# Performance work log

Hardware: AMD Instinct MI355X
Metric: run time of the kernel (lower is better)

## Reference

```python
import jax, jax.numpy as jnp
import numpy as np

# Module hyperparameters (init_kwargs)
D = 2          # input_dim
OUT = 3        # output_dim
T = 14         # log2 hash table size
L = 16         # number of levels
F = 2          # features per level
N_MIN, N_MAX = 16, 512
B = 1048576    # batch of query points
HIDDEN = 64

_b = np.exp((np.log(N_MAX) - np.log(N_MIN)) / (L - 1))
RES = jnp.asarray(np.floor(N_MIN * _b ** np.arange(L)).astype(np.float32))  # [L]

# voxel corner offsets [D, 2^D] (same construction as torch module)
_border = np.empty((D, 2 ** D), dtype=np.int32)
for _i in range(D):
    _border[_i, :] = np.array(([0] * 2 ** _i + [1] * 2 ** _i) * 2 ** (D - _i - 1), dtype=np.int32)
BORDER = jnp.asarray(_border)

# NVIDIA tiny-cuda-nn primes; uint32 arithmetic is exact for the low T bits
# (low 14 bits of a product/xor only depend on low 32 bits), matching torch's
# int64 multiply-xor followed by mod 2^T.
PRIMES = jnp.array([1, 2654435761, 805459861, 3674653429, 2097192037, 1434869437, 2165219737][:D], dtype=jnp.uint32)


def setup_inputs() -> dict:
    key = jax.random.key(0)
    ks = jax.random.split(key, 8)
    x = jax.random.uniform(ks[0], (B, D), jnp.float32)  # coords in [0,1)
    tables = jax.random.uniform(ks[1], (L, 2 ** T, F), jnp.float32, -1e-4, 1e-4)
    W1 = jax.random.normal(ks[2], (HIDDEN, L * F), jnp.float32) * 0.05
    b1 = jnp.zeros((HIDDEN,), jnp.float32)
    W2 = jax.random.normal(ks[3], (HIDDEN, HIDDEN), jnp.float32) * 0.05
    b2 = jnp.zeros((HIDDEN,), jnp.float32)
    W3 = jax.random.normal(ks[4], (OUT, HIDDEN), jnp.float32) * 0.05
    b3 = jnp.zeros((OUT,), jnp.float32)
    return {"x": x, "tables": tables, "W1": W1, "b1": b1, "W2": W2, "b2": b2, "W3": W3, "b3": b3}


def reference(x, tables, W1, b1, W2, b2, W3, b3):
    n = x.shape[0]
    # scale coords by each level resolution: [B, D, L]
    scaled = x[:, :, None] * RES[None, None, :]
    grid = jnp.floor(scaled).astype(jnp.int32)                     # [B, D, L]
    corners = grid[..., None] + BORDER[None, :, None, :]           # [B, D, L, 2^D]
    # spatial hash: xor of coord * prime per dimension, mod 2^T
    h = jnp.zeros((n, L, 2 ** D), jnp.uint32)
    for i in range(D):
        h = h ^ (corners[:, i].astype(jnp.uint32) * PRIMES[i])
    idx = (h & jnp.uint32(2 ** T - 1)).astype(jnp.int32)           # [B, L, 2^D]
    # per-level embedding gather: [B, L, 2^D, F]
    looked = tables[jnp.arange(L)[None, :, None], idx]
    # (bi/tri)linear interpolation weights: prod over dims -> [B, L, 2^D]
    w = jnp.prod(1.0 - jnp.abs(scaled[..., None] - corners.astype(x.dtype)), axis=1)
    feat = jnp.einsum('blc,blcf->blf', w, looked).reshape(n, L * F)  # [B, L*F]
    # small MLP head
    h1 = jax.nn.relu(feat @ W1.T + b1)
    h2 = jax.nn.relu(h1 @ W2.T + b2)
    return h2 @ W3.T + b3
```

## Files before the change

### kernel.cpp

```cpp
#include <hip/hip_runtime.h>
#include <hip/hip_bf16.h>
#include <math.h>


#define TBL_MASK 16383u
#define PRIME1   2654435761u

typedef __attribute__((ext_vector_type(8))) short short8;
typedef __attribute__((ext_vector_type(4))) float f32x4;
typedef __attribute__((ext_vector_type(4))) unsigned int uint4v;

struct ResArr { float r[16]; };

__device__ __forceinline__ unsigned short bf16rn(float f) {
    __hip_bfloat16 h = __float2bfloat16(f);
    return __builtin_bit_cast(unsigned short, h);
}
__device__ __forceinline__ float bf16tof(unsigned short u) {
    unsigned int x = ((unsigned int)u) << 16;
    return __builtin_bit_cast(float, x);
}

__device__ __forceinline__ void splitW(const float* __restrict__ p,
                                       short8& hi, short8& lo) {
    const float4 w0 = *(const float4*)p;
    const float4 w1 = *(const float4*)(p + 4);
    float v[8] = {w0.x, w0.y, w0.z, w0.w, w1.x, w1.y, w1.z, w1.w};
    #pragma unroll
    for (int e = 0; e < 8; ++e) {
        const unsigned short hb = bf16rn(v[e]);
        const unsigned short lb = bf16rn(v[e] - bf16tof(hb));
        hi[e] = (short)hb;
        lo[e] = (short)lb;
    }
}

__device__ __forceinline__ void splitWm(const float* __restrict__ p, bool valid,
                                        short8& hi, short8& lo) {
    float v[8];
    if (valid) {
        const float4 w0 = *(const float4*)p;
        const float4 w1 = *(const float4*)(p + 4);
        v[0] = w0.x; v[1] = w0.y; v[2] = w0.z; v[3] = w0.w;
        v[4] = w1.x; v[5] = w1.y; v[6] = w1.z; v[7] = w1.w;
    } else {
        #pragma unroll
        for (int e = 0; e < 8; ++e) v[e] = 0.0f;
    }
    #pragma unroll
    for (int e = 0; e < 8; ++e) {
        const unsigned short hb = bf16rn(v[e]);
        const unsigned short lb = bf16rn(v[e] - bf16tof(hb));
        hi[e] = (short)hb;
        lo[e] = (short)lb;
    }
}

__device__ __forceinline__ short8 ldsFrag(const unsigned short* p) {
    return __builtin_bit_cast(short8, *(const uint4v*)p);
}

#define MFMA(a, b, c) __builtin_amdgcn_mfma_f32_16x16x32_bf16((a), (b), (c), 0, 0, 0)

__global__ __launch_bounds__(64) void mh_mfma(
    const float* __restrict__ x,
    const float* __restrict__ tables,
    const float* __restrict__ W1,
    const float* __restrict__ b1,
    const float* __restrict__ W2,
    const float* __restrict__ b2,
    const float* __restrict__ W3,
    const float* __restrict__ b3,
    float* __restrict__ out,
    ResArr res, int n)
{
    __shared__ unsigned short sFH[64 * 40];
    __shared__ unsigned short sFL[64 * 40];
    __shared__ unsigned short sAH[32 * 72];
    __shared__ unsigned short sAL[32 * 72];

    const int L  = threadIdx.x;
    const int ln = L & 15;
    const int q  = L >> 4;
    const long base = (long)blockIdx.x * 64;
    long s = base + L;
    if (s >= (long)n) s = (long)n - 1;

    const float2 xv = reinterpret_cast<const float2*>(x)[s];
    const float2* __restrict__ tbl2 = reinterpret_cast<const float2*>(tables);

    #pragma unroll 4
    for (int l = 0; l < 16; ++l) {
        const float r  = res.r[l];
        const float sx = xv.x * r;
        const float sy = xv.y * r;
        const float gx = floorf(sx);
        const float gy = floorf(sy);
        const unsigned ux = (unsigned)(int)gx;
        const unsigned uy = (unsigned)(int)gy;
        const unsigned hy0 = uy * PRIME1;
        const unsigned hy1 = hy0 + PRIME1;
        const unsigned i00 = ( ux       ^ hy0) & TBL_MASK;
        const unsigned i10 = ((ux + 1u) ^ hy0) & TBL_MASK;
        const unsigned i01 = ( ux       ^ hy1) & TBL_MASK;
        const unsigned i11 = ((ux + 1u) ^ hy1) & TBL_MASK;
        const float2* tl = tbl2 + (l << 14);
        const float2 t00 = tl[i00];
        const float2 t10 = tl[i10];
        const float2 t01 = tl[i01];
        const float2 t11 = tl[i11];
        const float wx0 = 1.0f - fabsf(sx - gx);
        const float wx1 = 1.0f - fabsf(sx - (gx + 1.0f));
        const float wy0 = 1.0f - fabsf(sy - gy);
        const float wy1 = 1.0f - fabsf(sy - (gy + 1.0f));
        const float w00 = wx0 * wy0;
        const float w10 = wx1 * wy0;
        const float w01 = wx0 * wy1;
        const float w11 = wx1 * wy1;
        const float f0 = fmaf(w00, t00.x, fmaf(w10, t10.x, fmaf(w01, t01.x, w11 * t11.x)));
        const float f1 = fmaf(w00, t00.y, fmaf(w10, t10.y, fmaf(w01, t01.y, w11 * t11.y)));
        const unsigned short h0 = bf16rn(f0);
        const unsigned short h1e = bf16rn(f1);
        const unsigned short l0 = bf16rn(f0 - bf16tof(h0));
        const unsigned short l1 = bf16rn(f1 - bf16tof(h1e));
        *(unsigned int*)&sFH[L * 40 + 2 * l] = (unsigned)h0 | ((unsigned)h1e << 16);
        *(unsigned int*)&sFL[L * 40 + 2 * l] = (unsigned)l0 | ((unsigned)l1 << 16);
    }

    float b1v[4], b2v[4];
    #pragma unroll
    for (int nt = 0; nt < 4; ++nt) { b1v[nt] = b1[nt * 16 + ln]; b2v[nt] = b2[nt * 16 + ln]; }
    const float b3v = (ln < 3) ? b3[ln] : 0.0f;

    const f32x4 zero4 = {0.0f, 0.0f, 0.0f, 0.0f};

    for (int mh = 0; mh < 2; ++mh) {
        short8 a1h[2], a1l[2];
        #pragma unroll
        for (int mt = 0; mt < 2; ++mt) {
            const int row = mh * 32 + mt * 16 + ln;
            a1h[mt] = ldsFrag(&sFH[row * 40 + q * 8]);
            a1l[mt] = ldsFrag(&sFL[row * 40 + q * 8]);
        }
        f32x4 acc1[2][4];
        #pragma unroll
        for (int mt = 0; mt < 2; ++mt)
            #pragma unroll
            for (int nt = 0; nt < 4; ++nt) acc1[mt][nt] = zero4;

        #pragma unroll
        for (int nt = 0; nt < 4; ++nt) {
            short8 bh, bl;
            splitW(W1 + (nt * 16 + ln) * 32 + q * 8, bh, bl);
            #pragma unroll
            for (int mt = 0; mt < 2; ++mt) {
                f32x4 a = acc1[mt][nt];
                a = MFMA(a1l[mt], bh, a);
                a = MFMA(a1h[mt], bl, a);
                a = MFMA(a1h[mt], bh, a);
                acc1[mt][nt] = a;
            }
        }
        #pragma unroll
        for (int mt = 0; mt < 2; ++mt)
            #pragma unroll
            for (int nt = 0; nt < 4; ++nt) {
                const int col = nt * 16 + ln;
                #pragma unroll
                for (int r = 0; r < 4; ++r) {
                    float v = fmaxf(acc1[mt][nt][r] + b1v[nt], 0.0f);
                    const unsigned short hb = bf16rn(v);
                    const unsigned short lb = bf16rn(v - bf16tof(hb));
                    const int rl = mt * 16 + q * 4 + r;
                    sAH[rl * 72 + col] = hb;
                    sAL[rl * 72 + col] = lb;
                }
            }

        short8 a2h[2][2], a2l[2][2];
        #pragma unroll
        for (int mt = 0; mt < 2; ++mt)
            #pragma unroll
            for (int ks = 0; ks < 2; ++ks) {
                const int row = mt * 16 + ln;
                a2h[mt][ks] = ldsFrag(&sAH[row * 72 + ks * 32 + q * 8]);
                a2l[mt][ks] = ldsFrag(&sAL[row * 72 + ks * 32 + q * 8]);
            }
        f32x4 acc2[2][4];
        #pragma unroll
        for (int mt = 0; mt < 2; ++mt)
            #pragma unroll
            for (int nt = 0; nt < 4; ++nt) acc2[mt][nt] = zero4;

        #pragma unroll
        for (int nt = 0; nt < 4; ++nt)
            #pragma unroll
            for (int ks = 0; ks < 2; ++ks) {
                short8 bh, bl;
                splitW(W2 + (nt * 16 + ln) * 64 + ks * 32 + q * 8, bh, bl);
                #pragma unroll
                for (int mt = 0; mt < 2; ++mt) {
                    f32x4 a = acc2[mt][nt];
                    a = MFMA(a2l[mt][ks], bh, a);
                    a = MFMA(a2h[mt][ks], bl, a);
                    a = MFMA(a2h[mt][ks], bh, a);
                    acc2[mt][nt] = a;
                }
            }
        #pragma unroll
        for (int mt = 0; mt < 2; ++mt)
            #pragma unroll
            for (int nt = 0; nt < 4; ++nt) {
                const int col = nt * 16 + ln;
                #pragma unroll
                for (int r = 0; r < 4; ++r) {
                    float v = fmaxf(acc2[mt][nt][r] + b2v[nt], 0.0f);
                    const unsigned short hb = bf16rn(v);
                    const unsigned short lb = bf16rn(v - bf16tof(hb));
                    const int rl = mt * 16 + q * 4 + r;
                    sAH[rl * 72 + col] = hb;
                    sAL[rl * 72 + col] = lb;
                }
            }

        short8 a3h[2][2], a3l[2][2];
        #pragma unroll
        for (int mt = 0; mt < 2; ++mt)
            #pragma unroll
            for (int ks = 0; ks < 2; ++ks) {
                const int row = mt * 16 + ln;
                a3h[mt][ks] = ldsFrag(&sAH[row * 72 + ks * 32 + q * 8]);
                a3l[mt][ks] = ldsFrag(&sAL[row * 72 + ks * 32 + q * 8]);
            }
        f32x4 acc3[2] = {zero4, zero4};
        #pragma unroll
        for (int ks = 0; ks < 2; ++ks) {
            short8 bh, bl;
            splitWm(W3 + ln * 64 + ks * 32 + q * 8, ln < 3, bh, bl);
            #pragma unroll
            for (int mt = 0; mt < 2; ++mt) {
                f32x4 a = acc3[mt];
                a = MFMA(a3l[mt][ks], bh, a);
                a = MFMA(a3h[mt][ks], bl, a);
                a = MFMA(a3h[mt][ks], bh, a);
                acc3[mt] = a;
            }
        }
        if (ln < 3) {
            #pragma unroll
            for (int mt = 0; mt < 2; ++mt)
                #pragma unroll
                for (int r = 0; r < 4; ++r) {
                    const long sg = base + mh * 32 + mt * 16 + q * 4 + r;
                    if (sg < (long)n) out[sg * 3 + ln] = acc3[mt][r] + b3v;
                }
        }
    }
}

extern "C" void kernel_launch(void* const* d_in, const int* in_sizes, int n_in,
                              void* d_out, int out_size, void* d_ws, size_t ws_size,
                              hipStream_t stream) {
    const float* x      = (const float*)d_in[0];
    const float* tables = (const float*)d_in[1];
    const float* W1     = (const float*)d_in[2];
    const float* b1v    = (const float*)d_in[3];
    const float* W2     = (const float*)d_in[4];
    const float* b2v    = (const float*)d_in[5];
    const float* W3     = (const float*)d_in[6];
    const float* b3v    = (const float*)d_in[7];
    float* out = (float*)d_out;

    const int n = in_sizes[0] / 2;

    ResArr ra;
    const double bb = exp((log(512.0) - log(16.0)) / 15.0);
    for (int k = 0; k < 16; ++k) ra.r[k] = (float)floor(16.0 * pow(bb, (double)k));

    dim3 grid((n + 63) / 64), block(64);
    hipLaunchKernelGGL(mh_mfma, grid, block, 0, stream,
                       x, tables, W1, b1v, W2, b2v, W3, b3v, out, ra, n);
}
```

Baseline: 238.6 us.

## Pre-split MLP weights into bf16 hi/lo in a prep kernel

A small prep kernel now converts W1, W2 and W3 once per call into bf16 hi/lo pairs in workspace (W3 zero-padded to 16 rows). The main kernel then loads ready fragments instead of re-splitting the weights in every block, which removes a large amount of per-block VALU conversion work. Shared memory is aliased between the feature and activation buffers, with the feature fragments hoisted into registers beforehand. The encoding loop unroll is raised to 8. The cost is an extra launch and added register pressure.

Measured after the change: 255.7 us. 7.1% more time.

```diff
diff --git a/kernel.cpp b/kernel.cpp
--- a/kernel.cpp
+++ b/kernel.cpp
@@ -12,6 +12,13 @@
 
 struct ResArr { float r[16]; };
 
+#define WS_W1H 0
+#define WS_W1L 2048
+#define WS_W2H 4096
+#define WS_W2L 8192
+#define WS_W3H 12288
+#define WS_W3L 13312
+
 __device__ __forceinline__ unsigned short bf16rn(float f) {
     __hip_bfloat16 h = __float2bfloat16(f);
     return __builtin_bit_cast(unsigned short, h);
@@ -20,64 +27,54 @@
     unsigned int x = ((unsigned int)u) << 16;
     return __builtin_bit_cast(float, x);
 }
-
-__device__ __forceinline__ void splitW(const float* __restrict__ p,
-                                       short8& hi, short8& lo) {
-    const float4 w0 = *(const float4*)p;
-    const float4 w1 = *(const float4*)(p + 4);
-    float v[8] = {w0.x, w0.y, w0.z, w0.w, w1.x, w1.y, w1.z, w1.w};
-    #pragma unroll
-    for (int e = 0; e < 8; ++e) {
-        const unsigned short hb = bf16rn(v[e]);
-        const unsigned short lb = bf16rn(v[e] - bf16tof(hb));
-        hi[e] = (short)hb;
-        lo[e] = (short)lb;
+__device__ __forceinline__ short8 ldFrag(const unsigned short* p) {
+    return __builtin_bit_cast(short8, *(const uint4v*)p);
+}
+
+#define MFMA(a, b, c) __builtin_amdgcn_mfma_f32_16x16x32_bf16((a), (b), (c), 0, 0, 0)
+
+__global__ __launch_bounds__(256) void prep_weights(
+    const float* __restrict__ W1,
+    const float* __restrict__ W2,
+    const float* __restrict__ W3,
+    unsigned short* __restrict__ ws)
+{
+    const int t = blockIdx.x * 256 + threadIdx.x;
+    if (t < 2048) {
+        const float v = W1[t];
+        const unsigned short hb = bf16rn(v);
+        ws[WS_W1H + t] = hb;
+        ws[WS_W1L + t] = bf16rn(v - bf16tof(hb));
+    } else if (t < 2048 + 4096) {
+        const int i = t - 2048;
+        const float v = W2[i];
+        const unsigned short hb = bf16rn(v);
+        ws[WS_W2H + i] = hb;
+        ws[WS_W2L + i] = bf16rn(v - bf16tof(hb));
+    } else if (t < 2048 + 4096 + 1024) {
+        const int i = t - 6144;
+        const int r = i >> 6, c = i & 63;
+        const float v = (r < 3) ? W3[r * 64 + c] : 0.0f;
+        const unsigned short hb = bf16rn(v);
+        ws[WS_W3H + i] = hb;
+        ws[WS_W3L + i] = bf16rn(v - bf16tof(hb));
     }
 }
-
-__device__ __forceinline__ void splitWm(const float* __restrict__ p, bool valid,
-                                        short8& hi, short8& lo) {
-    float v[8];
-    if (valid) {
-        const float4 w0 = *(const float4*)p;
-        const float4 w1 = *(const float4*)(p + 4);
-        v[0] = w0.x; v[1] = w0.y; v[2] = w0.z; v[3] = w0.w;
-        v[4] = w1.x; v[5] = w1.y; v[6] = w1.z; v[7] = w1.w;
-    } else {
-        #pragma unroll
-        for (int e = 0; e < 8; ++e) v[e] = 0.0f;
-    }
-    #pragma unroll
-    for (int e = 0; e < 8; ++e) {
-        const unsigned short hb = bf16rn(v[e]);
-        const unsigned short lb = bf16rn(v[e] - bf16tof(hb));
-        hi[e] = (short)hb;
-        lo[e] = (short)lb;
-    }
-}
-
-__device__ __forceinline__ short8 ldsFrag(const unsigned short* p) {
-    return __builtin_bit_cast(short8, *(const uint4v*)p);
-}
-
-#define MFMA(a, b, c) __builtin_amdgcn_mfma_f32_16x16x32_bf16((a), (b), (c), 0, 0, 0)
 
 __global__ __launch_bounds__(64) void mh_mfma(
     const float* __restrict__ x,
     const float* __restrict__ tables,
-    const float* __restrict__ W1,
     const float* __restrict__ b1,
-    const float* __restrict__ W2,
     const float* __restrict__ b2,
-    const float* __restrict__ W3,
     const float* __restrict__ b3,
+    const unsigned short* __restrict__ ws,
     float* __restrict__ out,
     ResArr res, int n)
 {
-    __shared__ unsigned short sFH[64 * 40];
-    __shared__ unsigned short sFL[64 * 40];
-    __shared__ unsigned short sAH[32 * 72];
-    __shared__ unsigned short sAL[32 * 72];
+    __shared__ char smem[10240];
+    unsigned short* sF  = (unsigned short*)smem;
+    unsigned short* sAH = (unsigned short*)smem;
+    unsigned short* sAL = (unsigned short*)(smem + 4608);
 
     const int L  = threadIdx.x;
     const int ln = L & 15;
@@ -89,7 +86,7 @@
     const float2 xv = reinterpret_cast<const float2*>(x)[s];
     const float2* __restrict__ tbl2 = reinterpret_cast<const float2*>(tables);
 
-    #pragma unroll 4
+    #pragma unroll 8
     for (int l = 0; l < 16; ++l) {
         const float r  = res.r[l];
         const float sx = xv.x * r;
@@ -123,9 +120,19 @@
         const unsigned short h1e = bf16rn(f1);
         const unsigned short l0 = bf16rn(f0 - bf16tof(h0));
         const unsigned short l1 = bf16rn(f1 - bf16tof(h1e));
-        *(unsigned int*)&sFH[L * 40 + 2 * l] = (unsigned)h0 | ((unsigned)h1e << 16);
-        *(unsigned int*)&sFL[L * 40 + 2 * l] = (unsigned)l0 | ((unsigned)l1 << 16);
+        *(unsigned int*)&sF[L * 40 + 2 * l]        = (unsigned)h0 | ((unsigned)h1e << 16);
+        *(unsigned int*)&sF[2560 + L * 40 + 2 * l] = (unsigned)l0 | ((unsigned)l1 << 16);
     }
+
+    short8 fah[2][2], fal[2][2];
+    #pragma unroll
+    for (int mh = 0; mh < 2; ++mh)
+        #pragma unroll
+        for (int mt = 0; mt < 2; ++mt) {
+            const int row = mh * 32 + mt * 16 + ln;
+            fah[mh][mt] = ldFrag(&sF[row * 40 + q * 8]);
+            fal[mh][mt] = ldFrag(&sF[2560 + row * 40 + q * 8]);
+        }
 
     float b1v[4], b2v[4];
     #pragma unroll
@@ -135,13 +142,6 @@
     const f32x4 zero4 = {0.0f, 0.0f, 0.0f, 0.0f};
 
     for (int mh = 0; mh < 2; ++mh) {
-        short8 a1h[2], a1l[2];
-        #pragma unroll
-        for (int mt = 0; mt < 2; ++mt) {
-            const int row = mh * 32 + mt * 16 + ln;
-            a1h[mt] = ldsFrag(&sFH[row * 40 + q * 8]);
-            a1l[mt] = ldsFrag(&sFL[row * 40 + q * 8]);
-        }
         f32x4 acc1[2][4];
         #pragma unroll
         for (int mt = 0; mt < 2; ++mt)
@@ -150,14 +150,15 @@
 
         #pragma unroll
         for (int nt = 0; nt < 4; ++nt) {
-            short8 bh, bl;
-            splitW(W1 + (nt * 16 + ln) * 32 + q * 8, bh, bl);
+            const int off = (nt * 16 + ln) * 32 + q * 8;
+            const short8 bh = ldFrag(ws + WS_W1H + off);
+            const short8 bl = ldFrag(ws + WS_W1L + off);
             #pragma unroll
             for (int mt = 0; mt < 2; ++mt) {
                 f32x4 a = acc1[mt][nt];
-                a = MFMA(a1l[mt], bh, a);
-                a = MFMA(a1h[mt], bl, a);
-                a = MFMA(a1h[mt], bh, a);
+                a = MFMA(fal[mh][mt], bh, a);
+                a = MFMA(fah[mh][mt], bl, a);
+                a = MFMA(fah[mh][mt], bh, a);
                 acc1[mt][nt] = a;
             }
         }
@@ -183,8 +184,8 @@
             #pragma unroll
             for (int ks = 0; ks < 2; ++ks) {
                 const int row = mt * 16 + ln;
-                a2h[mt][ks] = ldsFrag(&sAH[row * 72 + ks * 32 + q * 8]);
-                a2l[mt][ks] = ldsFrag(&sAL[row * 72 + ks * 32 + q * 8]);
+                a2h[mt][ks] = ldFrag(&sAH[row * 72 + ks * 32 + q * 8]);
+                a2l[mt][ks] = ldFrag(&sAL[row * 72 + ks * 32 + q * 8]);
             }
         f32x4 acc2[2][4];
         #pragma unroll
@@ -196,8 +197,9 @@
         for (int nt = 0; nt < 4; ++nt)
             #pragma unroll
             for (int ks = 0; ks < 2; ++ks) {
-                short8 bh, bl;
-                splitW(W2 + (nt * 16 + ln) * 64 + ks * 32 + q * 8, bh, bl);
+                const int off = (nt * 16 + ln) * 64 + ks * 32 + q * 8;
+                const short8 bh = ldFrag(ws + WS_W2H + off);
+                const short8 bl = ldFrag(ws + WS_W2L + off);
                 #pragma unroll
                 for (int mt = 0; mt < 2; ++mt) {
                     f32x4 a = acc2[mt][nt];
@@ -229,14 +231,15 @@
             #pragma unroll
             for (int ks = 0; ks < 2; ++ks) {
                 const int row = mt * 16 + ln;
-                a3h[mt][ks] = ldsFrag(&sAH[row * 72 + ks * 32 + q * 8]);
-                a3l[mt][ks] = ldsFrag(&sAL[row * 72 + ks * 32 + q * 8]);
+                a3h[mt][ks] = ldFrag(&sAH[row * 72 + ks * 32 + q * 8]);
+                a3l[mt][ks] = ldFrag(&sAL[row * 72 + ks * 32 + q * 8]);
             }
         f32x4 acc3[2] = {zero4, zero4};
         #pragma unroll
         for (int ks = 0; ks < 2; ++ks) {
-            short8 bh, bl;
-            splitWm(W3 + ln * 64 + ks * 32 + q * 8, ln < 3, bh, bl);
+            const int off = ln * 64 + ks * 32 + q * 8;
+            const short8 bh = ldFrag(ws + WS_W3H + off);
+            const short8 bl = ldFrag(ws + WS_W3L + off);
             #pragma unroll
             for (int mt = 0; mt < 2; ++mt) {
                 f32x4 a = acc3[mt];
@@ -270,6 +273,7 @@
     const float* W3     = (const float*)d_in[6];
     const float* b3v    = (const float*)d_in[7];
     float* out = (float*)d_out;
+    unsigned short* ws = (unsigned short*)d_ws;
 
     const int n = in_sizes[0] / 2;
 
@@ -277,7 +281,7 @@
     const double bb = exp((log(512.0) - log(16.0)) / 15.0);
     for (int k = 0; k < 16; ++k) ra.r[k] = (float)floor(16.0 * pow(bb, (double)k));
 
-    dim3 grid((n + 63) / 64), block(64);
-    hipLaunchKernelGGL(mh_mfma, grid, block, 0, stream,
-                       x, tables, W1, b1v, W2, b2v, W3, b3v, out, ra, n);
-}
+    hipLaunchKernelGGL(prep_weights, dim3(28), dim3(256), 0, stream, W1, W2, W3, ws);
+    hipLaunchKernelGGL(mh_mfma, dim3((n + 63) / 64), dim3(64), 0, stream,
+                       x, tables, b1v, b2v, b3v, ws, out, ra, n);
+}
```
